# Performance work log

Hardware: AMD Instinct MI355X
Metric: run time of the kernel (lower is better)

## Reference

```python
import jax, jax.numpy as jnp
import numpy as np
import math

B, T, E, H = 4, 1024, 1024, 16
HD = E // H  # 64, even -> rope_dim == head_dim, no pass-through
SCALE = HD ** -0.5
PI = math.pi


def setup_inputs() -> dict:
    key = jax.random.key(0)
    ks = jax.random.split(key, 16)
    d = {}
    d["x_real"] = jax.random.normal(ks[0], (B, T, E), jnp.float32)
    d["x_imag"] = jax.random.normal(ks[1], (B, T, E), jnp.float32)
    d["lat"] = jax.random.uniform(ks[2], (B, T), jnp.float32) * 180.0
    d["lon"] = jax.random.uniform(ks[3], (B, T), jnp.float32) * 360.0
    i = 4
    for p in ("q", "k", "v", "o"):
        d[p + "_log_mag"] = jax.random.normal(ks[i], (E, E), jnp.float32) * 0.1; i += 1
        d[p + "_phase"] = jax.random.uniform(ks[i], (E, E), jnp.float32, minval=-PI, maxval=PI); i += 1
        d[p + "_bmag"] = jnp.zeros((E,), jnp.float32)
        d[p + "_bphase"] = jnp.zeros((E,), jnp.float32)
    d["dist_scale"] = jax.random.normal(ks[i], (H,), jnp.float32) * 0.1 - 0.5; i += 1
    d["dist_offset"] = jnp.zeros((H,), jnp.float32)
    return d


def _clinear(xr, xi, log_mag, phase, bmag, bphase):
    # Complex linear with magnitude-phase weights: W = exp(log_mag) * e^{i*phase}
    mag = jnp.exp(log_mag)
    wr = mag * jnp.cos(phase)
    wi = mag * jnp.sin(phase)
    r = xr @ wr.T - xi @ wi.T + bmag * jnp.cos(bphase)
    im = xr @ wi.T + xi @ wr.T + bmag * jnp.sin(bphase)
    return r, im


def _rotate_half(x):
    x1, x2 = jnp.split(x, 2, axis=-1)
    return jnp.concatenate([-x2, x1], axis=-1)


def _rope(xr, xi, cos_full, sin_full):
    # applied identically to real and imag parts (head_dim even -> full rope)
    r = xr * cos_full + _rotate_half(xr) * sin_full
    im = xi * cos_full + _rotate_half(xi) * sin_full
    return r, im


def _heads(x):  # [B,T,E] -> [B,H,T,HD]
    return x.reshape(B, T, H, HD).transpose(0, 2, 1, 3)


def _forward(x_real, x_imag, lat, lon,
             q_log_mag, q_phase, q_bmag, q_bphase,
             k_log_mag, k_phase, k_bmag, k_bphase,
             v_log_mag, v_phase, v_bmag, v_bphase,
             o_log_mag, o_phase, o_bmag, o_bphase,
             dist_scale, dist_offset):
    qr, qi = _clinear(x_real, x_imag, q_log_mag, q_phase, q_bmag, q_bphase)
    kr, ki = _clinear(x_real, x_imag, k_log_mag, k_phase, k_bmag, k_bphase)
    vr, vi = _clinear(x_real, x_imag, v_log_mag, v_phase, v_bmag, v_bphase)
    qr, qi, kr, ki, vr, vi = map(_heads, (qr, qi, kr, ki, vr, vi))

    # complex RoPE cache
    pos = jnp.arange(T, dtype=jnp.float32)
    inv_freq = 1.0 / (10000.0 ** (jnp.arange(0, HD, 2, dtype=jnp.float32) / HD))
    freqs = pos[:, None] * inv_freq[None, :]          # [T, HD/2]
    cos = jnp.cos(freqs); sin = jnp.sin(freqs)
    cos_full = jnp.concatenate([cos, cos], -1)[None, None]  # [1,1,T,HD]
    sin_full = jnp.concatenate([sin, sin], -1)[None, None]
    qr, qi = _rope(qr, qi, cos_full, sin_full)
    kr, ki = _rope(kr, ki, cos_full, sin_full)

    # Hermitian attention scores: Re(Q K^H) = Re(Q)Re(K)^T + Im(Q)Im(K)^T
    scores = (jnp.einsum('bhqd,bhkd->bhqk', qr, kr)
              + jnp.einsum('bhqd,bhkd->bhqk', qi, ki)) * SCALE

    # spatial attention bias via haversine distance
    lat_rad = (lat - 90.0) / 180.0 * PI
    lon_rad = lon / 360.0 * (2.0 * PI)
    lat1 = lat_rad[:, :, None]; lat2 = lat_rad[:, None, :]   # [B,T,1],[B,1,T]
    dlat = lat2 - lat1
    dlon = lon_rad[:, None, :] - lon_rad[:, :, None]
    a = jnp.sin(dlat / 2) ** 2 + jnp.cos(lat1) * jnp.cos(lat2) * jnp.sin(dlon / 2) ** 2
    dist_deg = 2.0 * jnp.arcsin(jnp.sqrt(jnp.clip(a, 0.0, 1.0))) * (180.0 / PI)
    log_dist = jnp.log1p(dist_deg)[:, None]                  # [B,1,T,T]
    bias = dist_scale[None, :, None, None] * log_dist + dist_offset[None, :, None, None]
    scores = scores + bias

    # causal mask (block_size == T)
    causal = jnp.tril(jnp.ones((T, T), dtype=bool))
    scores = jnp.where(causal[None, None], scores, jnp.float32(-1e9))
    attn = jax.nn.softmax(scores, axis=-1)

    # complex value aggregation: real attention weights times complex V
    or_ = jnp.einsum('bhqk,bhkd->bhqd', attn, vr)
    oi_ = jnp.einsum('bhqk,bhkd->bhqd', attn, vi)
    or_ = or_.transpose(0, 2, 1, 3).reshape(B, T, E)
    oi_ = oi_.transpose(0, 2, 1, 3).reshape(B, T, E)

    yr, yi = _clinear(or_, oi_, o_log_mag, o_phase, o_bmag, o_bphase)
    return jnp.stack([yr, yi])  # [2,B,T,E] (real, imag)


def reference(x_real, x_imag, lat, lon,
              q_log_mag, q_phase, q_bmag, q_bphase,
              k_log_mag, k_phase, k_bmag, k_bphase,
              v_log_mag, v_phase, v_bmag, v_bphase,
              o_log_mag, o_phase, o_bmag, o_bphase,
              dist_scale, dist_offset):
    return _forward(x_real, x_imag, lat, lon,
                    q_log_mag, q_phase, q_bmag, q_bphase,
                    k_log_mag, k_phase, k_bmag, k_bphase,
                    v_log_mag, v_phase, v_bmag, v_bphase,
                    o_log_mag, o_phase, o_bmag, o_bphase,
                    dist_scale, dist_offset)
```

## Files before the change

kernel.cpp:

```cpp
#include <hip/hip_runtime.h>
#include <math.h>

#define B_ 4
#define T_ 1024
#define E_ 1024
#define H_ 16
#define HD_ 64

constexpr float SCALE_ = 0.125f;
constexpr float PI_F = 3.14159265358979323846f;

constexpr size_t BTE = (size_t)B_ * T_ * E_;
constexpr size_t BTT = (size_t)B_ * T_ * T_;
constexpr int M_ = B_ * T_;
constexpr int KC_ = 2 * E_;

typedef __attribute__((ext_vector_type(8))) short bf16x8;
typedef __attribute__((ext_vector_type(4))) float f32x4;

__device__ __forceinline__ short f2bf(float f) {
    unsigned int u = __float_as_uint(f);
    unsigned int r = (u + 0x7fffu + ((u >> 16) & 1u)) >> 16;
    return (short)r;
}
__device__ __forceinline__ float bf2f(short s) {
    return __uint_as_float(((unsigned int)(unsigned short)s) << 16);
}
__device__ __forceinline__ void fsplit(float v, short& h, short& l) {
    short hh = f2bf(v);
    h = hh;
    l = f2bf(v - bf2f(hh));
}
__device__ __forceinline__ void gl_lds16(const void* g, void* l) {
    __builtin_amdgcn_global_load_lds(
        (const __attribute__((address_space(1))) unsigned int*)g,
        (__attribute__((address_space(3))) unsigned int*)l, 16, 0, 0);
}

__global__ __launch_bounds__(256) void wgen(const float* __restrict__ lm,
                                            const float* __restrict__ ph,
                                            short* __restrict__ W) {
    int idx = blockIdx.x * 256 + threadIdx.x;
    int n = idx >> 10, k = idx & 1023;
    float m = expf(lm[idx]);
    float s, c;
    sincosf(ph[idx], &s, &c);
    float wr = m * c, wi = m * s;
    size_t r0 = (size_t)n * KC_;
    size_t r1 = (size_t)(n + 1024) * KC_;
    W[r0 + k]        = f2bf(wr);
    W[r0 + 1024 + k] = f2bf(-wi);
    W[r1 + k]        = f2bf(wi);
    W[r1 + 1024 + k] = f2bf(wr);
}

__global__ __launch_bounds__(256) void wgen_split(const float* __restrict__ lm,
                                                  const float* __restrict__ ph,
                                                  short* __restrict__ Wh,
                                                  short* __restrict__ Wl) {
    int idx = blockIdx.x * 256 + threadIdx.x;
    int n = idx >> 10, k = idx & 1023;
    float m = expf(lm[idx]);
    float s, c;
    sincosf(ph[idx], &s, &c);
    float wr = m * c, wi = m * s;
    size_t o0 = (size_t)n * KC_ + k;
    size_t o1 = (size_t)n * KC_ + 1024 + k;
    size_t o2 = (size_t)(n + 1024) * KC_ + k;
    size_t o3 = (size_t)(n + 1024) * KC_ + 1024 + k;
    short h, l;
    fsplit(wr,  h, l); Wh[o0] = h; Wl[o0] = l;
    fsplit(-wi, h, l); Wh[o1] = h; Wl[o1] = l;
    fsplit(wi,  h, l); Wh[o2] = h; Wl[o2] = l;
    fsplit(wr,  h, l); Wh[o3] = h; Wl[o3] = l;
}

__global__ __launch_bounds__(256) void xcat_split(const float* __restrict__ xr,
                                                  const float* __restrict__ xi,
                                                  short* __restrict__ xh,
                                                  short* __restrict__ xl) {
    size_t idx = (size_t)blockIdx.x * 256 + threadIdx.x;
    size_t m = idx >> 10, k = idx & 1023;
    short h, l;
    fsplit(xr[idx], h, l);
    xh[m * KC_ + k] = h; xl[m * KC_ + k] = l;
    fsplit(xi[idx], h, l);
    xh[m * KC_ + 1024 + k] = h; xl[m * KC_ + 1024 + k] = l;
}

__global__ __launch_bounds__(256) void geodist(const float* __restrict__ lat,
                                               const float* __restrict__ lon,
                                               float* __restrict__ ld) {
    size_t idx = (size_t)blockIdx.x * 256 + threadIdx.x;
    int k = (int)(idx & (T_ - 1));
    int q = (int)((idx >> 10) & (T_ - 1));
    int b = (int)(idx >> 20);
    float la1 = (lat[b * T_ + q] - 90.f) * (PI_F / 180.f);
    float la2 = (lat[b * T_ + k] - 90.f) * (PI_F / 180.f);
    float lo1 = lon[b * T_ + q] * (PI_F / 180.f);
    float lo2 = lon[b * T_ + k] * (PI_F / 180.f);
    float sdla = sinf((la2 - la1) * 0.5f);
    float sdlo = sinf((lo2 - lo1) * 0.5f);
    float a = sdla * sdla + cosf(la1) * cosf(la2) * sdlo * sdlo;
    a = fminf(fmaxf(a, 0.f), 1.f);
    float dd = 2.f * asinf(sqrtf(a)) * (180.f / PI_F);
    ld[idx] = log1pf(dd);
}

__global__ __launch_bounds__(256) void cgemm_qk(const short* __restrict__ Ah,
                                                const short* __restrict__ Al,
                                                const short* __restrict__ Wh,
                                                const short* __restrict__ Wl,
                                                const float* __restrict__ bmag,
                                                const float* __restrict__ bphase,
                                                short* __restrict__ Qh,
                                                short* __restrict__ Ql) {
    __shared__ short sAh[128 * 32], sAl[128 * 32];
    __shared__ short sBh[128 * 32], sBl[128 * 32];

    const int tid = threadIdx.x;
    const int w = tid >> 6, l = tid & 63;
    const int wm = w >> 1, wn = w & 1;
    const int wl = l & 15, g = l >> 4;

    int id = blockIdx.y * 32 + blockIdx.x;
    int swz = (id & 7) * 64 + (id >> 3);
    const int bm = (swz & 31) * 128;
    const int bn = (swz >> 5) * 128;

    f32x4 acc[4][4];
#pragma unroll
    for (int m = 0; m < 4; ++m)
#pragma unroll
        for (int n = 0; n < 4; ++n) acc[m][n] = (f32x4){0.f, 0.f, 0.f, 0.f};

    for (int k0 = 0; k0 < KC_; k0 += 32) {
        __syncthreads();
#pragma unroll
        for (int i = 0; i < 2; ++i) {
            int chunk = (w * 2 + i) * 64 + l;
            int row = chunk >> 2, kc = chunk & 3;
            size_t ga = (size_t)(bm + row) * KC_ + k0 + kc * 8;
            size_t gb = (size_t)(bn + row) * KC_ + k0 + kc * 8;
            gl_lds16(Ah + ga, sAh + (w * 2 + i) * 64 * 8);
            gl_lds16(Al + ga, sAl + (w * 2 + i) * 64 * 8);
            gl_lds16(Wh + gb, sBh + (w * 2 + i) * 64 * 8);
            gl_lds16(Wl + gb, sBl + (w * 2 + i) * 64 * 8);
        }
        __syncthreads();

        bf16x8 afh[4], afl[4], bfh[4], bfl[4];
#pragma unroll
        for (int m = 0; m < 4; ++m) {
            afh[m] = *(const bf16x8*)&sAh[(wm * 64 + m * 16 + wl) * 32 + g * 8];
            afl[m] = *(const bf16x8*)&sAl[(wm * 64 + m * 16 + wl) * 32 + g * 8];
        }
#pragma unroll
        for (int n = 0; n < 4; ++n) {
            bfh[n] = *(const bf16x8*)&sBh[(wn * 64 + n * 16 + wl) * 32 + g * 8];
            bfl[n] = *(const bf16x8*)&sBl[(wn * 64 + n * 16 + wl) * 32 + g * 8];
        }
#pragma unroll
        for (int m = 0; m < 4; ++m)
#pragma unroll
            for (int n = 0; n < 4; ++n) {
                acc[m][n] = __builtin_amdgcn_mfma_f32_16x16x32_bf16(afh[m], bfh[n], acc[m][n], 0, 0, 0);
                acc[m][n] = __builtin_amdgcn_mfma_f32_16x16x32_bf16(afh[m], bfl[n], acc[m][n], 0, 0, 0);
                acc[m][n] = __builtin_amdgcn_mfma_f32_16x16x32_bf16(afl[m], bfh[n], acc[m][n], 0, 0, 0);
            }
    }

#pragma unroll
    for (int n = 0; n < 4; ++n) {
        const int col = bn + wn * 64 + n * 16 + wl;
        const int ch = col & 1023;
        float sb, cb;
        sincosf(bphase[ch], &sb, &cb);
        const float bias = bmag[ch] * (col < 1024 ? cb : sb);
#pragma unroll
        for (int m = 0; m < 4; ++m)
#pragma unroll
            for (int r = 0; r < 4; ++r) acc[m][n][r] += bias;
    }

#pragma unroll
    for (int n = 0; n < 2; ++n) {
        const int j = n * 16 + wl;
        const float invf = expf(-(2.f * j / 64.f) * 9.210340371976184f);
#pragma unroll
        for (int m = 0; m < 4; ++m)
#pragma unroll
            for (int r = 0; r < 4; ++r) {
                const int row = bm + wm * 64 + m * 16 + g * 4 + r;
                const float th = (float)(row & 1023) * invf;
                float s_, c_;
                sincosf(th, &s_, &c_);
                const float x1 = acc[m][n][r], x2 = acc[m][n + 2][r];
                acc[m][n][r]     = x1 * c_ - x2 * s_;
                acc[m][n + 2][r] = x2 * c_ + x1 * s_;
            }
    }

#pragma unroll
    for (int n = 0; n < 4; ++n) {
        const int col = bn + wn * 64 + n * 16 + wl;
        const int ch = col & 1023;
        const int off = (ch >> 6) * 128 + (ch & 63) + ((col >= 1024) ? 64 : 0);
#pragma unroll
        for (int m = 0; m < 4; ++m)
#pragma unroll
            for (int r = 0; r < 4; ++r) {
                const int row = bm + wm * 64 + m * 16 + g * 4 + r;
                short h_, l_;
                fsplit(acc[m][n][r], h_, l_);
                Qh[(size_t)row * KC_ + off] = h_;
                Ql[(size_t)row * KC_ + off] = l_;
            }
    }
}

__global__ __launch_bounds__(256) void cgemm_mfma(const short* __restrict__ A,
                                                  const short* __restrict__ W,
                                                  const float* __restrict__ bmag,
                                                  const float* __restrict__ bphase,
                                                  short* __restrict__ outbf,
                                                  float* __restrict__ outr,
                                                  float* __restrict__ outi,
                                                  int mode) {
    __shared__ short sA[128 * 32];
    __shared__ short sB[128 * 32];

    const int tid = threadIdx.x;
    const int w = tid >> 6, l = tid & 63;
    const int wm = w >> 1, wn = w & 1;
    const int wl = l & 15, g = l >> 4;

    int id = blockIdx.y * 32 + blockIdx.x;
    int swz = (id & 7) * 64 + (id >> 3);
    const int bm = (swz & 31) * 128;
    const int bn = (swz >> 5) * 128;

    f32x4 acc[4][4];
#pragma unroll
    for (int m = 0; m < 4; ++m)
#pragma unroll
        for (int n = 0; n < 4; ++n) acc[m][n] = (f32x4){0.f, 0.f, 0.f, 0.f};

    for (int k0 = 0; k0 < KC_; k0 += 32) {
        __syncthreads();
#pragma unroll
        for (int i = 0; i < 2; ++i) {
            int chunk = (w * 2 + i) * 64 + l;
            int row = chunk >> 2, kc = chunk & 3;
            gl_lds16(A + (size_t)(bm + row) * KC_ + k0 + kc * 8, sA + (w * 2 + i) * 64 * 8);
            gl_lds16(W + (size_t)(bn + row) * KC_ + k0 + kc * 8, sB + (w * 2 + i) * 64 * 8);
        }
        __syncthreads();

        bf16x8 af[4], bfr[4];
#pragma unroll
        for (int m = 0; m < 4; ++m)
            af[m] = *(const bf16x8*)&sA[(wm * 64 + m * 16 + wl) * 32 + g * 8];
#pragma unroll
        for (int n = 0; n < 4; ++n)
            bfr[n] = *(const bf16x8*)&sB[(wn * 64 + n * 16 + wl) * 32 + g * 8];
#pragma unroll
        for (int m = 0; m < 4; ++m)
#pragma unroll
            for (int n = 0; n < 4; ++n)
                acc[m][n] = __builtin_amdgcn_mfma_f32_16x16x32_bf16(af[m], bfr[n], acc[m][n], 0, 0, 0);
    }

#pragma unroll
    for (int n = 0; n < 4; ++n) {
        const int col = bn + wn * 64 + n * 16 + wl;
        const int ch = col & 1023;
        float sb, cb;
        sincosf(bphase[ch], &sb, &cb);
        const float bias = bmag[ch] * (col < 1024 ? cb : sb);
#pragma unroll
        for (int m = 0; m < 4; ++m) {
#pragma unroll
            for (int r = 0; r < 4; ++r) {
                const int row = bm + wm * 64 + m * 16 + g * 4 + r;
                const float v = acc[m][n][r] + bias;
                if (mode == 0) {
                    const int hh = ch >> 6, d = ch & 63;
                    outbf[(size_t)row * KC_ + hh * 128 + d + ((col >= 1024) ? 64 : 0)] = f2bf(v);
                } else {
                    if (col < 1024) outr[(size_t)row * E_ + col] = v;
                    else            outi[(size_t)row * E_ + (col - 1024)] = v;
                }
            }
        }
    }
}

__global__ __launch_bounds__(256) void attn_split(const short* __restrict__ qh,
                                                  const short* __restrict__ ql,
                                                  const short* __restrict__ kh,
                                                  const short* __restrict__ kl,
                                                  const short* __restrict__ vc,
                                                  const float* __restrict__ ld,
                                                  const float* __restrict__ dsc,
                                                  const float* __restrict__ dof,
                                                  short* __restrict__ otc) {
    __shared__ short sKh[64 * 128];
    __shared__ short sKl[64 * 128];
    __shared__ short sV[2][64 * 66];
    __shared__ short sP[4][16 * 68];

    const int qt = blockIdx.x, h = blockIdx.y, b = blockIdx.z;
    const int tid = threadIdx.x;
    const int w = tid >> 6, l = tid & 63;
    const int wl = l & 15, g = l >> 4;

    const float dsch = dsc[h], dofh = dof[h];

    bf16x8 aqh[4], aql[4];
    {
        const size_t qbase = ((size_t)(b * T_) + qt * 64 + w * 16 + wl) * KC_ + h * 128;
#pragma unroll
        for (int ks = 0; ks < 4; ++ks) {
            aqh[ks] = *(const bf16x8*)(qh + qbase + ks * 32 + g * 8);
            aql[ks] = *(const bf16x8*)(ql + qbase + ks * 32 + g * 8);
        }
    }

    f32x4 accR[4], accI[4];
#pragma unroll
    for (int nb = 0; nb < 4; ++nb) {
        accR[nb] = (f32x4){0.f, 0.f, 0.f, 0.f};
        accI[nb] = (f32x4){0.f, 0.f, 0.f, 0.f};
    }
    float m_run[4], l_run[4];
#pragma unroll
    for (int r = 0; r < 4; ++r) { m_run[r] = -3.0e38f; l_run[r] = 0.f; }

    for (int kt = 0; kt <= qt; ++kt) {
        __syncthreads();

#pragma unroll
        for (int i = 0; i < 4; ++i) {
            int chunk = (w * 4 + i) * 64 + l;
            int row = chunk >> 4;
            int c8 = (chunk & 15) ^ ((row & 7) << 1);
            size_t src = ((size_t)(b * T_) + kt * 64 + row) * KC_ + h * 128 + c8 * 8;
            gl_lds16(kh + src, sKh + (w * 4 + i) * 64 * 8);
            gl_lds16(kl + src, sKl + (w * 4 + i) * 64 * 8);
        }
        {
            const short* vrow = vc + ((size_t)(b * T_) + kt * 64 + l) * KC_ + h * 128;
#pragma unroll
            for (int comp = 0; comp < 2; ++comp)
#pragma unroll
                for (int half = 0; half < 2; ++half) {
                    int d0 = w * 8 + half * 32;
                    bf16x8 v8 = *(const bf16x8*)(vrow + comp * 64 + d0);
#pragma unroll
                    for (int j = 0; j < 8; ++j) sV[comp][(d0 + j) * 66 + l] = v8[j];
                }
        }
        __syncthreads();

        f32x4 s[4];
#pragma unroll
        for (int nb = 0; nb < 4; ++nb) s[nb] = (f32x4){0.f, 0.f, 0.f, 0.f};
#pragma unroll
        for (int nb = 0; nb < 4; ++nb) {
            const int ktl = nb * 16 + wl;
#pragma unroll
            for (int ks = 0; ks < 4; ++ks) {
                const int pc8 = (ks * 4 + g) ^ ((ktl & 7) << 1);
                const bf16x8 bkh = *(const bf16x8*)&sKh[ktl * 128 + pc8 * 8];
                const bf16x8 bkl = *(const bf16x8*)&sKl[ktl * 128 + pc8 * 8];
                s[nb] = __builtin_amdgcn_mfma_f32_16x16x32_bf16(aqh[ks], bkh, s[nb], 0, 0, 0);
                s[nb] = __builtin_amdgcn_mfma_f32_16x16x32_bf16(aqh[ks], bkl, s[nb], 0, 0, 0);
                s[nb] = __builtin_amdgcn_mfma_f32_16x16x32_bf16(aql[ks], bkh, s[nb], 0, 0, 0);
            }
        }

        const int qg0 = qt * 64 + w * 16 + g * 4;
        const int kg0 = kt * 64;
#pragma unroll
        for (int nb = 0; nb < 4; ++nb) {
            const int kg = kg0 + nb * 16 + wl;
            const float* ldp = ld + ((size_t)b * T_ + qg0) * T_ + kg;
#pragma unroll
            for (int r = 0; r < 4; ++r) {
                float sv = s[nb][r] * SCALE_ + dsch * ldp[(size_t)r * T_] + dofh;
                if (kt == qt && kg > qg0 + r) sv = -1.0e9f;
                s[nb][r] = sv;
            }
        }

#pragma unroll
        for (int r = 0; r < 4; ++r) {
            float mt = fmaxf(fmaxf(s[0][r], s[1][r]), fmaxf(s[2][r], s[3][r]));
            mt = fmaxf(mt, __shfl_xor(mt, 1));
            mt = fmaxf(mt, __shfl_xor(mt, 2));
            mt = fmaxf(mt, __shfl_xor(mt, 4));
            mt = fmaxf(mt, __shfl_xor(mt, 8));
            const float mnew = fmaxf(m_run[r], mt);
            const float sc = __expf(m_run[r] - mnew);
            m_run[r] = mnew;
            float rs = 0.f;
#pragma unroll
            for (int nb = 0; nb < 4; ++nb) {
                const float p = __expf(s[nb][r] - mnew);
                s[nb][r] = p;
                rs += p;
            }
            rs += __shfl_xor(rs, 1);
            rs += __shfl_xor(rs, 2);
            rs += __shfl_xor(rs, 4);
            rs += __shfl_xor(rs, 8);
            l_run[r] = l_run[r] * sc + rs;
#pragma unroll
            for (int nb = 0; nb < 4; ++nb) { accR[nb][r] *= sc; accI[nb][r] *= sc; }
        }

#pragma unroll
        for (int nb = 0; nb < 4; ++nb)
#pragma unroll
            for (int r = 0; r < 4; ++r)
                sP[w][(g * 4 + r) * 68 + nb * 16 + wl] = f2bf(s[nb][r]);

        bf16x8 ap[2];
#pragma unroll
        for (int ks = 0; ks < 2; ++ks)
            ap[ks] = *(const bf16x8*)&sP[w][wl * 68 + ks * 32 + g * 8];
#pragma unroll
        for (int nb = 0; nb < 4; ++nb) {
#pragma unroll
            for (int ks = 0; ks < 2; ++ks) {
                const bf16x8 bvr = *(const bf16x8*)&sV[0][(nb * 16 + wl) * 66 + ks * 32 + g * 8];
                const bf16x8 bvi = *(const bf16x8*)&sV[1][(nb * 16 + wl) * 66 + ks * 32 + g * 8];
                accR[nb] = __builtin_amdgcn_mfma_f32_16x16x32_bf16(ap[ks], bvr, accR[nb], 0, 0, 0);
                accI[nb] = __builtin_amdgcn_mfma_f32_16x16x32_bf16(ap[ks], bvi, accI[nb], 0, 0, 0);
            }
        }
    }

    float inv[4];
#pragma unroll
    for (int r = 0; r < 4; ++r) inv[r] = 1.0f / l_run[r];
#pragma unroll
    for (int nb = 0; nb < 4; ++nb) {
#pragma unroll
        for (int r = 0; r < 4; ++r) {
            const int q = qt * 64 + w * 16 + g * 4 + r;
            const int d = nb * 16 + wl;
            const size_t base = ((size_t)(b * T_) + q) * KC_ + h * 64 + d;
            otc[base] = f2bf(accR[nb][r] * inv[r]);
            otc[base + 1024] = f2bf(accI[nb][r] * inv[r]);
        }
    }
}

extern "C" void kernel_launch(void* const* d_in, const int* in_sizes, int n_in,
                              void* d_out, int out_size, void* d_ws, size_t ws_size,
                              hipStream_t stream) {
    const float* x_r  = (const float*)d_in[0];
    const float* x_i  = (const float*)d_in[1];
    const float* lat  = (const float*)d_in[2];
    const float* lon  = (const float*)d_in[3];
    const float* q_lm = (const float*)d_in[4];
    const float* q_ph = (const float*)d_in[5];
    const float* q_bm = (const float*)d_in[6];
    const float* q_bp = (const float*)d_in[7];
    const float* k_lm = (const float*)d_in[8];
    const float* k_ph = (const float*)d_in[9];
    const float* k_bm = (const float*)d_in[10];
    const float* k_bp = (const float*)d_in[11];
    const float* v_lm = (const float*)d_in[12];
    const float* v_ph = (const float*)d_in[13];
    const float* v_bm = (const float*)d_in[14];
    const float* v_bp = (const float*)d_in[15];
    const float* o_lm = (const float*)d_in[16];
    const float* o_ph = (const float*)d_in[17];
    const float* o_bm = (const float*)d_in[18];
    const float* o_bp = (const float*)d_in[19];
    const float* dsc  = (const float*)d_in[20];
    const float* dof  = (const float*)d_in[21];

    char* ws = (char*)d_ws;
    const size_t MB = 1024u * 1024u;
    short* Wv  = (short*)(ws + 0 * MB);
    short* Wo  = (short*)(ws + 8 * MB);
    short* Wqh = (short*)(ws + 16 * MB);
    short* Wql = (short*)(ws + 24 * MB);
    short* Wkh = (short*)(ws + 32 * MB);
    short* Wkl = (short*)(ws + 40 * MB);
    short* xch = (short*)(ws + 48 * MB);
    short* xcl = (short*)(ws + 64 * MB);
    short* qhh = (short*)(ws + 80 * MB);
    short* qll = (short*)(ws + 96 * MB);
    short* khh = (short*)(ws + 112 * MB);
    short* kll = (short*)(ws + 128 * MB);
    short* vcb = (short*)(ws + 144 * MB);
    short* otc = (short*)(ws + 160 * MB);
    float* ldt = (float*)(ws + 176 * MB);

    wgen_split<<<(E_ * E_) / 256, 256, 0, stream>>>(q_lm, q_ph, Wqh, Wql);
    wgen_split<<<(E_ * E_) / 256, 256, 0, stream>>>(k_lm, k_ph, Wkh, Wkl);
    wgen<<<(E_ * E_) / 256, 256, 0, stream>>>(v_lm, v_ph, Wv);
    wgen<<<(E_ * E_) / 256, 256, 0, stream>>>(o_lm, o_ph, Wo);
    xcat_split<<<BTE / 256, 256, 0, stream>>>(x_r, x_i, xch, xcl);
    geodist<<<BTT / 256, 256, 0, stream>>>(lat, lon, ldt);

    dim3 ggrid(M_ / 128, KC_ / 128);
    cgemm_qk<<<ggrid, 256, 0, stream>>>(xch, xcl, Wqh, Wql, q_bm, q_bp, qhh, qll);
    cgemm_qk<<<ggrid, 256, 0, stream>>>(xch, xcl, Wkh, Wkl, k_bm, k_bp, khh, kll);
    cgemm_mfma<<<ggrid, 256, 0, stream>>>(xch, Wv, v_bm, v_bp, vcb, nullptr, nullptr, 0);

    dim3 agrid(T_ / 64, H_, B_);
    attn_split<<<agrid, 256, 0, stream>>>(qhh, qll, khh, kll, vcb, ldt, dsc, dof, otc);

    float* yr = (float*)d_out;
    float* yi = (float*)d_out + BTE;
    cgemm_mfma<<<ggrid, 256, 0, stream>>>(otc, Wo, o_bm, o_bp, nullptr, yr, yi, 1);
}
```

Measured before the change: 737.1 us.

## Widen attention blocks to 128 queries, balance causal scheduling, store geo bias as bf16

The attention kernel now uses 512 threads (8 waves) per block covering 128 query rows, so each K/V tile loaded to shared memory is reused by twice as many queries. The grid is flattened to 512 blocks, and query tiles are ordered so that long and short causal rows are interleaved to balance load. The log-distance bias table is stored as bf16 instead of fp32, halving its memory traffic in both the producer and the attention kernel. The cost is a slight precision loss in the bias and higher register and shared-memory pressure per block.

```diff
diff --git a/kernel.cpp b/kernel.cpp
--- a/kernel.cpp
+++ b/kernel.cpp
@@ -90,7 +90,7 @@
 
 __global__ __launch_bounds__(256) void geodist(const float* __restrict__ lat,
                                                const float* __restrict__ lon,
-                                               float* __restrict__ ld) {
+                                               short* __restrict__ ld) {
     size_t idx = (size_t)blockIdx.x * 256 + threadIdx.x;
     int k = (int)(idx & (T_ - 1));
     int q = (int)((idx >> 10) & (T_ - 1));
@@ -104,7 +104,7 @@
     float a = sdla * sdla + cosf(la1) * cosf(la2) * sdlo * sdlo;
     a = fminf(fmaxf(a, 0.f), 1.f);
     float dd = 2.f * asinf(sqrtf(a)) * (180.f / PI_F);
-    ld[idx] = log1pf(dd);
+    ld[idx] = f2bf(log1pf(dd));
 }
 
 __global__ __launch_bounds__(256) void cgemm_qk(const short* __restrict__ Ah,
@@ -296,21 +296,27 @@
     }
 }
 
-__global__ __launch_bounds__(256) void attn_split(const short* __restrict__ qh,
+__global__ __launch_bounds__(512) void attn_split(const short* __restrict__ qh,
                                                   const short* __restrict__ ql,
                                                   const short* __restrict__ kh,
                                                   const short* __restrict__ kl,
                                                   const short* __restrict__ vc,
-                                                  const float* __restrict__ ld,
+                                                  const short* __restrict__ ldb,
                                                   const float* __restrict__ dsc,
                                                   const float* __restrict__ dof,
                                                   short* __restrict__ otc) {
     __shared__ short sKh[64 * 128];
     __shared__ short sKl[64 * 128];
     __shared__ short sV[2][64 * 66];
-    __shared__ short sP[4][16 * 68];
-
-    const int qt = blockIdx.x, h = blockIdx.y, b = blockIdx.z;
+    __shared__ short sP[8][16 * 68];
+
+    const int j = blockIdx.x;
+    const int h = j & 15;
+    const int idx = j >> 4;
+    const int b = idx & 3;
+    const int q4 = idx >> 2;
+    const int qt = (q4 < 4) ? (7 - q4) : (q4 - 4);
+
     const int tid = threadIdx.x;
     const int w = tid >> 6, l = tid & 63;
     const int wl = l & 15, g = l >> 4;
@@ -319,7 +325,7 @@
 
     bf16x8 aqh[4], aql[4];
     {
-        const size_t qbase = ((size_t)(b * T_) + qt * 64 + w * 16 + wl) * KC_ + h * 128;
+        const size_t qbase = ((size_t)(b * T_) + qt * 128 + w * 16 + wl) * KC_ + h * 128;
 #pragma unroll
         for (int ks = 0; ks < 4; ++ks) {
             aqh[ks] = *(const bf16x8*)(qh + qbase + ks * 32 + g * 8);
@@ -337,29 +343,29 @@
 #pragma unroll
     for (int r = 0; r < 4; ++r) { m_run[r] = -3.0e38f; l_run[r] = 0.f; }
 
-    for (int kt = 0; kt <= qt; ++kt) {
+    const int nkt = 2 * qt + 2;
+    for (int kt = 0; kt < nkt; ++kt) {
         __syncthreads();
 
 #pragma unroll
-        for (int i = 0; i < 4; ++i) {
-            int chunk = (w * 4 + i) * 64 + l;
+        for (int i = 0; i < 2; ++i) {
+            int chunk = (w * 2 + i) * 64 + l;
             int row = chunk >> 4;
             int c8 = (chunk & 15) ^ ((row & 7) << 1);
             size_t src = ((size_t)(b * T_) + kt * 64 + row) * KC_ + h * 128 + c8 * 8;
-            gl_lds16(kh + src, sKh + (w * 4 + i) * 64 * 8);
-            gl_lds16(kl + src, sKl + (w * 4 + i) * 64 * 8);
+            gl_lds16(kh + src, sKh + (w * 2 + i) * 64 * 8);
+            gl_lds16(kl + src, sKl + (w * 2 + i) * 64 * 8);
         }
         {
             const short* vrow = vc + ((size_t)(b * T_) + kt * 64 + l) * KC_ + h * 128;
-#pragma unroll
-            for (int comp = 0; comp < 2; ++comp)
-#pragma unroll
-                for (int half = 0; half < 2; ++half) {
-                    int d0 = w * 8 + half * 32;
-                    bf16x8 v8 = *(const bf16x8*)(vrow + comp * 64 + d0);
-#pragma unroll
-                    for (int j = 0; j < 8; ++j) sV[comp][(d0 + j) * 66 + l] = v8[j];
-                }
+            const int comp = w >> 2;
+            const int d0 = (w & 3) * 16;
+#pragma unroll
+            for (int half = 0; half < 2; ++half) {
+                bf16x8 v8 = *(const bf16x8*)(vrow + comp * 64 + d0 + half * 8);
+#pragma unroll
+                for (int jj = 0; jj < 8; ++jj) sV[comp][(d0 + half * 8 + jj) * 66 + l] = v8[jj];
+            }
         }
         __syncthreads();
 
@@ -380,16 +386,17 @@
             }
         }
 
-        const int qg0 = qt * 64 + w * 16 + g * 4;
+        const int qg0 = qt * 128 + w * 16 + g * 4;
         const int kg0 = kt * 64;
+        const bool domask = (kt >= 2 * qt);
 #pragma unroll
         for (int nb = 0; nb < 4; ++nb) {
             const int kg = kg0 + nb * 16 + wl;
-            const float* ldp = ld + ((size_t)b * T_ + qg0) * T_ + kg;
+            const short* ldp = ldb + ((size_t)b * T_ + qg0) * T_ + kg;
 #pragma unroll
             for (int r = 0; r < 4; ++r) {
-                float sv = s[nb][r] * SCALE_ + dsch * ldp[(size_t)r * T_] + dofh;
-                if (kt == qt && kg > qg0 + r) sv = -1.0e9f;
+                float sv = s[nb][r] * SCALE_ + dsch * bf2f(ldp[(size_t)r * T_]) + dofh;
+                if (domask && kg > qg0 + r) sv = -1.0e9f;
                 s[nb][r] = sv;
             }
         }
@@ -449,7 +456,7 @@
     for (int nb = 0; nb < 4; ++nb) {
 #pragma unroll
         for (int r = 0; r < 4; ++r) {
-            const int q = qt * 64 + w * 16 + g * 4 + r;
+            const int q = qt * 128 + w * 16 + g * 4 + r;
             const int d = nb * 16 + wl;
             const size_t base = ((size_t)(b * T_) + q) * KC_ + h * 64 + d;
             otc[base] = f2bf(accR[nb][r] * inv[r]);
@@ -500,7 +507,7 @@
     short* kll = (short*)(ws + 128 * MB);
     short* vcb = (short*)(ws + 144 * MB);
     short* otc = (short*)(ws + 160 * MB);
-    float* ldt = (float*)(ws + 176 * MB);
+    short* ldt = (short*)(ws + 176 * MB);
 
     wgen_split<<<(E_ * E_) / 256, 256, 0, stream>>>(q_lm, q_ph, Wqh, Wql);
     wgen_split<<<(E_ * E_) / 256, 256, 0, stream>>>(k_lm, k_ph, Wkh, Wkl);
@@ -514,8 +521,7 @@
     cgemm_qk<<<ggrid, 256, 0, stream>>>(xch, xcl, Wkh, Wkl, k_bm, k_bp, khh, kll);
     cgemm_mfma<<<ggrid, 256, 0, stream>>>(xch, Wv, v_bm, v_bp, vcb, nullptr, nullptr, 0);
 
-    dim3 agrid(T_ / 64, H_, B_);
-    attn_split<<<agrid, 256, 0, stream>>>(qhh, qll, khh, kll, vcb, ldt, dsc, dof, otc);
+    attn_split<<<512, 512, 0, stream>>>(qhh, qll, khh, kll, vcb, ldt, dsc, dof, otc);
 
     float* yr = (float*)d_out;
     float* yi = (float*)d_out + BTE;
```

Result: faster. 649.3 us (-11.9%).
